# Performance work log

Hardware: AMD Instinct MI355X
Metric: run time of the kernel (lower is better)

The kernel has to match this reference:

```python
import jax, jax.numpy as jnp
import numpy as np

B, S, D, H = 2, 2048, 1024, 16
DK = D // H


def setup_inputs() -> dict:
    key = jax.random.key(0)
    ks = jax.random.split(key, 12)
    scale = 1.0 / np.sqrt(D)
    inp = {
        "q": jax.random.normal(ks[0], (B, S, D), jnp.float32),
        "k": jax.random.normal(ks[1], (B, S, D), jnp.float32),
        "v": jax.random.normal(ks[2], (B, S, D), jnp.float32),
        # causal mask: 1 = attend, 0 = mask, broadcastable to (B, 1, S, S)
        "mask": jnp.tril(jnp.ones((S, S), jnp.int32))[None, None, :, :],
        "Wq": jax.random.normal(ks[3], (D, D), jnp.float32) * scale,
        "bq": jax.random.normal(ks[4], (D,), jnp.float32) * scale,
        "Wk": jax.random.normal(ks[5], (D, D), jnp.float32) * scale,
        "bk": jax.random.normal(ks[6], (D,), jnp.float32) * scale,
        "Wv": jax.random.normal(ks[7], (D, D), jnp.float32) * scale,
        "bv": jax.random.normal(ks[8], (D,), jnp.float32) * scale,
        "Wo": jax.random.normal(ks[9], (D, D), jnp.float32) * scale,
        "bo": jax.random.normal(ks[10], (D,), jnp.float32) * scale,
    }
    return inp


def _split_heads(x):
    b, s, _ = x.shape
    return x.reshape(b, s, H, DK).transpose(0, 2, 1, 3)  # (b, h, s, dk)


def reference(q, k, v, mask, Wq, bq, Wk, bk, Wv, bv, Wo, bo):
    Q = _split_heads(q @ Wq.T + bq)
    K = _split_heads(k @ Wk.T + bk)
    V = _split_heads(v @ Wv.T + bv)
    scores = jnp.einsum("bhqd,bhkd->bhqk", Q, K) * (DK ** -0.5)
    scores = jnp.where(mask == 0, -jnp.inf, scores)
    attn = jax.nn.softmax(scores, axis=-1)  # dropout p=0.0 -> identity
    out = jnp.einsum("bhqk,bhkd->bhqd", attn, V)
    out = out.transpose(0, 2, 1, 3).reshape(q.shape[0], q.shape[1], D)
    return out @ Wo.T + bo
```

## Files before the change

kernel.cpp:

```cpp
#include <hip/hip_runtime.h>


#define S_LEN 2048
#define NHEAD 16
#define DMODEL 1024
#define DKH 64
#define LDT 88

typedef unsigned short u16;
typedef __attribute__((ext_vector_type(4))) short short4v;
typedef __attribute__((ext_vector_type(8))) short short8;
typedef __attribute__((ext_vector_type(8))) __bf16 bf16x8;
typedef __attribute__((ext_vector_type(4))) float f32x4;

__device__ inline u16 f2bf(float f) {
  return __builtin_bit_cast(u16, (__bf16)f);
}

__device__ inline f32x4 mfma16x16(bf16x8 a, bf16x8 b, f32x4 c) {
  return __builtin_amdgcn_mfma_f32_16x16x32_bf16(a, b, c, 0, 0, 0);
}

__device__ inline short8 pack8(float4 a, float4 b) {
  short8 r;
  r[0] = (short)f2bf(a.x); r[1] = (short)f2bf(a.y);
  r[2] = (short)f2bf(a.z); r[3] = (short)f2bf(a.w);
  r[4] = (short)f2bf(b.x); r[5] = (short)f2bf(b.y);
  r[6] = (short)f2bf(b.z); r[7] = (short)f2bf(b.w);
  return r;
}

typedef const __attribute__((address_space(1))) unsigned GU32;
typedef __attribute__((address_space(3))) unsigned LU32;
__device__ inline void gl2lds16(const void* g, void* l) {
  __builtin_amdgcn_global_load_lds((GU32*)g, (LU32*)l, 16, 0, 0);
}

#define SWZ(row, col8) (((row) * 8 + ((col8) ^ ((row) & 7))) * 8)

__global__ __launch_bounds__(256)
void conv_bf16(const float* __restrict__ w0, const float* __restrict__ w1,
               const float* __restrict__ w2, const float* __restrict__ w3,
               const float* __restrict__ aq, const float* __restrict__ ak,
               const float* __restrict__ av,
               u16* __restrict__ o0, u16* __restrict__ o1,
               u16* __restrict__ o2, u16* __restrict__ o3,
               u16* __restrict__ oq, u16* __restrict__ ok, u16* __restrict__ ov)
{
  const int y = blockIdx.y;
  const float* s; u16* d; int n;
  switch (y) {
    case 0: s = w0; d = o0; n = 1 << 20; break;
    case 1: s = w1; d = o1; n = 1 << 20; break;
    case 2: s = w2; d = o2; n = 1 << 20; break;
    case 3: s = w3; d = o3; n = 1 << 20; break;
    case 4: s = aq; d = oq; n = 1 << 22; break;
    case 5: s = ak; d = ok; n = 1 << 22; break;
    default: s = av; d = ov; n = 1 << 22; break;
  }
  const int i = (blockIdx.x * 256 + threadIdx.x) * 8;
  if (i >= n) return;
  float4 a = *(const float4*)&s[i];
  float4 b = *(const float4*)&s[i + 4];
  *(short8*)&d[i] = pack8(a, b);
}

__global__ __launch_bounds__(256)
void conv_w(const float* __restrict__ w0, const float* __restrict__ w1,
            const float* __restrict__ w2, const float* __restrict__ w3,
            u16* __restrict__ o0, u16* __restrict__ o1,
            u16* __restrict__ o2, u16* __restrict__ o3)
{
  const int z = blockIdx.y;
  const float* s = z == 0 ? w0 : z == 1 ? w1 : z == 2 ? w2 : w3;
  u16* d = z == 0 ? o0 : z == 1 ? o1 : z == 2 ? o2 : o3;
  const int i = (blockIdx.x * 256 + threadIdx.x) * 8;
  float4 a = *(const float4*)&s[i];
  float4 b = *(const float4*)&s[i + 4];
  *(short8*)&d[i] = pack8(a, b);
}

__global__ __launch_bounds__(256)
void proj_gemm_bf16(const u16* __restrict__ Aqb, const u16* __restrict__ Akb,
                    const u16* __restrict__ Avb,
                    const u16* __restrict__ Bq, const u16* __restrict__ Bk,
                    const u16* __restrict__ Bv,
                    const float* __restrict__ cq, const float* __restrict__ ck,
                    const float* __restrict__ cv,
                    u16* __restrict__ Oq, u16* __restrict__ Ok, u16* __restrict__ Ov)
{
  __shared__ u16 SM[4 * 8192];

  const int hw = blockIdx.x + (blockIdx.y << 3) + (blockIdx.z << 8);
  const int xcd = hw & 7, sq = hw >> 3;
  const int pan = sq % 12, xb = sq / 12;
  const int p = pan * 8 + xcd;
  const int zz = p >> 5, py = p & 31;

  const u16* Ab = zz == 0 ? Aqb : zz == 1 ? Akb : Avb;
  const u16* Wb = zz == 0 ? Bq : zz == 1 ? Bk : Bv;
  const float* bias = zz == 0 ? cq : zz == 1 ? ck : cv;

  const int t = threadIdx.x;
  const int lane = t & 63;
  const int wv = t >> 6;
  const int wm = wv >> 1, wn = wv & 1;
  const int g = lane >> 4, lr = lane & 15;
  const int bm = py << 7, bn = xb << 7;
  const int K = DMODEL;

  auto STAGE = [&](int buf, int kt) {
    const int k0 = kt << 6;
    u16* Asb = SM + buf * 8192;
    u16* Bsb = SM + 16384 + buf * 8192;
#pragma unroll
    for (int i = 0; i < 4; ++i) {
      int c = t + (i << 8);
      int row = c >> 3, col8 = c & 7;
      int c8s = col8 ^ (row & 7);
      gl2lds16(&Ab[(size_t)(bm + row) * K + k0 + c8s * 8], &Asb[c * 8]);
      gl2lds16(&Wb[(size_t)(bn + row) * K + k0 + c8s * 8], &Bsb[c * 8]);
    }
  };

  f32x4 acc[4][4] = {};
  STAGE(0, 0);
  __syncthreads();
  for (int kt = 0; kt < 16; ++kt) {
    const int cur = kt & 1;
    if (kt + 1 < 16) STAGE(cur ^ 1, kt + 1);
    u16* Asb = SM + cur * 8192;
    u16* Bsb = SM + 16384 + cur * 8192;
    bf16x8 af[2][4], bf[2][4];
#pragma unroll
    for (int kc = 0; kc < 2; ++kc)
#pragma unroll
      for (int f = 0; f < 4; ++f) {
        af[kc][f] = *(const bf16x8*)&Asb[SWZ(wm * 64 + f * 16 + lr, kc * 4 + g)];
        bf[kc][f] = *(const bf16x8*)&Bsb[SWZ(wn * 64 + f * 16 + lr, kc * 4 + g)];
      }
#pragma unroll
    for (int kc = 0; kc < 2; ++kc)
#pragma unroll
      for (int fm = 0; fm < 4; ++fm)
#pragma unroll
        for (int fn = 0; fn < 4; ++fn)
          acc[fm][fn] = mfma16x16(af[kc][fm], bf[kc][fn], acc[fm][fn]);
    __syncthreads();
  }

  if (zz == 2) {
    u16* TL = SM;
    const int b = bm >> 11, s0 = bm & (S_LEN - 1), h0 = bn >> 6;
#pragma unroll
    for (int hh = 0; hh < 2; ++hh) {
      __syncthreads();
      if (wn == hh) {
#pragma unroll
        for (int fm = 0; fm < 4; ++fm)
#pragma unroll
          for (int fn = 0; fn < 4; ++fn) {
            const int lch = fn * 16 + lr;
            const float bb = bias[bn + hh * 64 + lch];
#pragma unroll
            for (int r = 0; r < 4; ++r)
              TL[lch * 132 + wm * 64 + fm * 16 + g * 4 + r] = f2bf(acc[fm][fn][r] + bb);
          }
      }
      __syncthreads();
#pragma unroll
      for (int i = 0; i < 4; ++i) {
        int c = t + (i << 8);
        int dk = c >> 4, sc = (c & 15) << 3;
        short8 vv = *(const short8*)&TL[dk * 132 + sc];
        *(short8*)&Ov[(((size_t)(b * NHEAD + h0 + hh)) * DKH + dk) * S_LEN + s0 + sc] = vv;
      }
    }
  } else {
    u16* Out = zz == 0 ? Oq : Ok;
#pragma unroll
    for (int fm = 0; fm < 4; ++fm)
#pragma unroll
      for (int fn = 0; fn < 4; ++fn) {
        const int col = bn + wn * 64 + fn * 16 + lr;
        const int h = col >> 6, dk = col & (DKH - 1);
        const float bb = bias[col];
#pragma unroll
        for (int r = 0; r < 4; ++r) {
          const int row = bm + wm * 64 + fm * 16 + g * 4 + r;
          const int b = row >> 11, s = row & (S_LEN - 1);
          Out[(((size_t)(b * NHEAD + h)) * S_LEN + s) * DKH + dk] = f2bf(acc[fm][fn][r] + bb);
        }
      }
  }
}

__global__ __launch_bounds__(256)
void proj_gemm_f32(const float* __restrict__ Aq, const float* __restrict__ Akk,
                   const float* __restrict__ Av,
                   const u16* __restrict__ Bq, const u16* __restrict__ Bk,
                   const u16* __restrict__ Bv,
                   const float* __restrict__ cq, const float* __restrict__ ck,
                   const float* __restrict__ cv,
                   u16* __restrict__ Oq, u16* __restrict__ Ok, u16* __restrict__ Ov)
{
  __shared__ u16 SM[3 * 8192];
  u16* As = SM;
  u16* Bs0 = SM + 8192;
  u16* Bs1 = SM + 16384;

  const int hw = blockIdx.x + (blockIdx.y << 3) + (blockIdx.z << 8);
  const int xcd = hw & 7, sq = hw >> 3;
  const int pan = sq % 12, xb = sq / 12;
  const int p = pan * 8 + xcd;
  const int zz = p >> 5, py = p & 31;

  const float* Af = zz == 0 ? Aq : zz == 1 ? Akk : Av;
  const u16* Wb = zz == 0 ? Bq : zz == 1 ? Bk : Bv;
  const float* bias = zz == 0 ? cq : zz == 1 ? ck : cv;

  const int t = threadIdx.x;
  const int lane = t & 63;
  const int wv = t >> 6;
  const int wm = wv >> 1, wn = wv & 1;
  const int g = lane >> 4, lr = lane & 15;
  const int bm = py << 7, bn = xb << 7;
  const int K = DMODEL;

  float4 ax[4], ay[4];
  auto ALOAD = [&](int kt) {
    const int k0 = kt << 6;
#pragma unroll
    for (int i = 0; i < 4; ++i) {
      int c = t + (i << 8);
      int row = c >> 3, col8 = c & 7;
      const float* src = &Af[(size_t)(bm + row) * K + k0 + col8 * 8];
      ax[i] = *(const float4*)src;
      ay[i] = *(const float4*)(src + 4);
    }
  };
  auto AWRITE = [&]() {
#pragma unroll
    for (int i = 0; i < 4; ++i) {
      int c = t + (i << 8);
      int row = c >> 3, col8 = c & 7;
      *(short8*)&As[SWZ(row, col8)] = pack8(ax[i], ay[i]);
    }
  };
  auto BSTAGE = [&](u16* buf, int kt) {
    const int k0 = kt << 6;
#pragma unroll
    for (int i = 0; i < 4; ++i) {
      int c = t + (i << 8);
      int row = c >> 3, col8 = c & 7;
      int c8s = col8 ^ (row & 7);
      gl2lds16(&Wb[(size_t)(bn + row) * K + k0 + c8s * 8], &buf[c * 8]);
    }
  };

  f32x4 acc[4][4] = {};
  ALOAD(0);
  BSTAGE(Bs0, 0);
  AWRITE();
  __syncthreads();
  for (int kt = 0; kt < 16; ++kt) {
    u16* Bcur = (kt & 1) ? Bs1 : Bs0;
    u16* Bnxt = (kt & 1) ? Bs0 : Bs1;
    const bool more = (kt + 1 < 16);
    if (more) { ALOAD(kt + 1); BSTAGE(Bnxt, kt + 1); }
    bf16x8 af[2][4], bf[2][4];
#pragma unroll
    for (int kc = 0; kc < 2; ++kc)
#pragma unroll
      for (int f = 0; f < 4; ++f) {
        af[kc][f] = *(const bf16x8*)&As[SWZ(wm * 64 + f * 16 + lr, kc * 4 + g)];
        bf[kc][f] = *(const bf16x8*)&Bcur[SWZ(wn * 64 + f * 16 + lr, kc * 4 + g)];
      }
#pragma unroll
    for (int kc = 0; kc < 2; ++kc)
#pragma unroll
      for (int fm = 0; fm < 4; ++fm)
#pragma unroll
        for (int fn = 0; fn < 4; ++fn)
          acc[fm][fn] = mfma16x16(af[kc][fm], bf[kc][fn], acc[fm][fn]);
    __syncthreads();
    if (more) {
      AWRITE();
      __syncthreads();
    }
  }

  if (zz == 2) {
    u16* TL = SM;
    const int b = bm >> 11, s0 = bm & (S_LEN - 1), h0 = bn >> 6;
#pragma unroll
    for (int hh = 0; hh < 2; ++hh) {
      __syncthreads();
      if (wn == hh) {
#pragma unroll
        for (int fm = 0; fm < 4; ++fm)
#pragma unroll
          for (int fn = 0; fn < 4; ++fn) {
            const int lch = fn * 16 + lr;
            const float bb = bias[bn + hh * 64 + lch];
#pragma unroll
            for (int r = 0; r < 4; ++r)
              TL[lch * 132 + wm * 64 + fm * 16 + g * 4 + r] = f2bf(acc[fm][fn][r] + bb);
          }
      }
      __syncthreads();
#pragma unroll
      for (int i = 0; i < 4; ++i) {
        int c = t + (i << 8);
        int dk = c >> 4, sc = (c & 15) << 3;
        short8 vv = *(const short8*)&TL[dk * 132 + sc];
        *(short8*)&Ov[(((size_t)(b * NHEAD + h0 + hh)) * DKH + dk) * S_LEN + s0 + sc] = vv;
      }
    }
  } else {
    u16* Out = zz == 0 ? Oq : Ok;
#pragma unroll
    for (int fm = 0; fm < 4; ++fm)
#pragma unroll
      for (int fn = 0; fn < 4; ++fn) {
        const int col = bn + wn * 64 + fn * 16 + lr;
        const int h = col >> 6, dk = col & (DKH - 1);
        const float bb = bias[col];
#pragma unroll
        for (int r = 0; r < 4; ++r) {
          const int row = bm + wm * 64 + fm * 16 + g * 4 + r;
          const int b = row >> 11, s = row & (S_LEN - 1);
          Out[(((size_t)(b * NHEAD + h)) * S_LEN + s) * DKH + dk] = f2bf(acc[fm][fn][r] + bb);
        }
      }
  }
}

__global__ __launch_bounds__(256)
void out_gemm(const u16* __restrict__ Ao, const u16* __restrict__ Wb,
              const float* __restrict__ bias, float* __restrict__ Out)
{
  __shared__ u16 SM[4 * 8192];
  const int hw = blockIdx.x + (blockIdx.y << 3);
  const int xcd = hw & 7, sq = hw >> 3;
  const int pan = sq & 3, xb = sq >> 2;
  const int prow = pan * 8 + xcd;

  const int t = threadIdx.x;
  const int lane = t & 63;
  const int wv = t >> 6;
  const int wm = wv >> 1, wn = wv & 1;
  const int g = lane >> 4, lr = lane & 15;
  const int bm = prow << 7, bn = xb << 7;
  const int K = DMODEL;

  auto STAGE = [&](int buf, int kt) {
    const int k0 = kt << 6;
    u16* Asb = SM + buf * 8192;
    u16* Bsb = SM + 16384 + buf * 8192;
#pragma unroll
    for (int i = 0; i < 4; ++i) {
      int c = t + (i << 8);
      int row = c >> 3, col8 = c & 7;
      int c8s = col8 ^ (row & 7);
      int grow = bm + row;
      int b = grow >> 11, s = grow & (S_LEN - 1);
      int k = k0 + c8s * 8;
      int h = k >> 6, dk = k & (DKH - 1);
      gl2lds16(&Ao[(((size_t)(b * NHEAD + h)) * S_LEN + s) * DKH + dk], &Asb[c * 8]);
      gl2lds16(&Wb[(size_t)(bn + row) * K + k0 + c8s * 8], &Bsb[c * 8]);
    }
  };

  f32x4 acc[4][4] = {};
  STAGE(0, 0);
  __syncthreads();
  for (int kt = 0; kt < 16; ++kt) {
    const int cur = kt & 1;
    if (kt + 1 < 16) STAGE(cur ^ 1, kt + 1);
    u16* Asb = SM + cur * 8192;
    u16* Bsb = SM + 16384 + cur * 8192;
    bf16x8 af[2][4], bf[2][4];
#pragma unroll
    for (int kc = 0; kc < 2; ++kc)
#pragma unroll
      for (int f = 0; f < 4; ++f) {
        af[kc][f] = *(const bf16x8*)&Asb[SWZ(wm * 64 + f * 16 + lr, kc * 4 + g)];
        bf[kc][f] = *(const bf16x8*)&Bsb[SWZ(wn * 64 + f * 16 + lr, kc * 4 + g)];
      }
#pragma unroll
    for (int kc = 0; kc < 2; ++kc)
#pragma unroll
      for (int fm = 0; fm < 4; ++fm)
#pragma unroll
        for (int fn = 0; fn < 4; ++fn)
          acc[fm][fn] = mfma16x16(af[kc][fm], bf[kc][fn], acc[fm][fn]);
    __syncthreads();
  }
#pragma unroll
  for (int fm = 0; fm < 4; ++fm)
#pragma unroll
    for (int fn = 0; fn < 4; ++fn) {
      const int col = bn + wn * 64 + fn * 16 + lr;
      const float bb = bias[col];
#pragma unroll
      for (int r = 0; r < 4; ++r) {
        const int row = bm + wm * 64 + fm * 16 + g * 4 + r;
        Out[(size_t)row * DMODEL + col] = acc[fm][fn][r] + bb;
      }
    }
}

__global__ __launch_bounds__(256)
void attn_fwd(const u16* __restrict__ Qh, const u16* __restrict__ Kh,
              const u16* __restrict__ Vtg, u16* __restrict__ Ao)
{
  __shared__ u16 Ks[2][64 * LDT];
  __shared__ u16 Vs[2][64 * LDT];
  __shared__ u16 Ps[8][16 * LDT];
  const int t = threadIdx.x, lane = t & 63, w = t >> 6;
  const int g = lane >> 4, lr = lane & 15;
  const int bh = blockIdx.y;
  const int pA = blockIdx.x;
  const int tA = pA, tB = 31 - pA;
  const u16* Qb = Qh + (size_t)bh * S_LEN * DKH;
  const u16* Kb = Kh + (size_t)bh * S_LEN * DKH;
  const u16* Vb = Vtg + (size_t)bh * DKH * S_LEN;

  bf16x8 qfA[2], qfB[2];
#pragma unroll
  for (int kc = 0; kc < 2; ++kc) {
    qfA[kc] = *(const bf16x8*)&Qb[(size_t)(tA * 64 + w * 16 + lr) * DKH + kc * 32 + g * 8];
    qfB[kc] = *(const bf16x8*)&Qb[(size_t)(tB * 64 + w * 16 + lr) * DKH + kc * 32 + g * 8];
  }

  f32x4 oA[4] = {}, oB[4] = {};
  float mA = -1e30f, lA = 0.f, mB = -1e30f, lB = 0.f;

  const int r0 = t >> 3;
  const int c0 = (t & 7) << 3;
  short8 kr0, kr1, vr0, vr1;

  auto LOADT = [&](int kt) {
    const int kv0 = kt << 6;
    kr0 = *(const short8*)&Kb[(size_t)(kv0 + r0) * DKH + c0];
    kr1 = *(const short8*)&Kb[(size_t)(kv0 + r0 + 32) * DKH + c0];
    vr0 = *(const short8*)&Vb[(size_t)r0 * S_LEN + kv0 + c0];
    vr1 = *(const short8*)&Vb[(size_t)(r0 + 32) * S_LEN + kv0 + c0];
  };
  auto WRITET = [&](int b) {
    *(short8*)&Ks[b][r0 * LDT + c0] = kr0;
    *(short8*)&Ks[b][(r0 + 32) * LDT + c0] = kr1;
    *(short8*)&Vs[b][r0 * LDT + c0] = vr0;
    *(short8*)&Vs[b][(r0 + 32) * LDT + c0] = vr1;
  };

  auto COMPUTE = [&](int buf, const bf16x8* qf, f32x4* o, float& m, float& l,
                     int pslot, bool diag) {
    f32x4 sf[4];
#pragma unroll
    for (int fk = 0; fk < 4; ++fk) {
      f32x4 a = {};
#pragma unroll
      for (int kc = 0; kc < 2; ++kc) {
        bf16x8 kf = *(const bf16x8*)&Ks[buf][(fk * 16 + lr) * LDT + kc * 32 + g * 8];
        a = mfma16x16(kf, qf[kc], a);
      }
      sf[fk] = a;
    }
    if (diag) {
#pragma unroll
      for (int fk = 0; fk < 4; ++fk)
#pragma unroll
        for (int r = 0; r < 4; ++r)
          if (fk * 16 + 4 * g + r > w * 16 + lr) sf[fk][r] = -1e30f;
    }
    float pm = fmaxf(fmaxf(sf[0][0], sf[0][1]), fmaxf(sf[0][2], sf[0][3]));
#pragma unroll
    for (int fk = 1; fk < 4; ++fk)
      pm = fmaxf(pm, fmaxf(fmaxf(sf[fk][0], sf[fk][1]), fmaxf(sf[fk][2], sf[fk][3])));
    pm = fmaxf(pm, __shfl_xor(pm, 16, 64));
    pm = fmaxf(pm, __shfl_xor(pm, 32, 64));
    float alpha = 1.0f;
    if (!__all(pm - m <= 64.0f)) {
      float mn = fmaxf(m, pm);
      alpha = __expf((m - mn) * 0.125f);
      m = mn;
#pragma unroll
      for (int r = 0; r < 4; ++r) {
        float ar = __shfl(alpha, 4 * g + r, 64);
#pragma unroll
        for (int d = 0; d < 4; ++d) o[d][r] *= ar;
      }
    }
    float rs = 0.f;
#pragma unroll
    for (int fk = 0; fk < 4; ++fk) {
      float p0 = __expf((sf[fk][0] - m) * 0.125f);
      float p1 = __expf((sf[fk][1] - m) * 0.125f);
      float p2 = __expf((sf[fk][2] - m) * 0.125f);
      float p3 = __expf((sf[fk][3] - m) * 0.125f);
      rs += (p0 + p1) + (p2 + p3);
      short4v pk;
      pk[0] = (short)f2bf(p0); pk[1] = (short)f2bf(p1);
      pk[2] = (short)f2bf(p2); pk[3] = (short)f2bf(p3);
      *(short4v*)&Ps[pslot][lr * LDT + fk * 16 + 4 * g] = pk;
    }
    rs += __shfl_xor(rs, 16, 64);
    rs += __shfl_xor(rs, 32, 64);
    l = l * alpha + rs;
#pragma unroll
    for (int kc = 0; kc < 2; ++kc) {
      bf16x8 pf = *(const bf16x8*)&Ps[pslot][lr * LDT + kc * 32 + g * 8];
#pragma unroll
      for (int df = 0; df < 4; ++df) {
        bf16x8 vf = *(const bf16x8*)&Vs[buf][(df * 16 + lr) * LDT + kc * 32 + g * 8];
        o[df] = mfma16x16(pf, vf, o[df]);
      }
    }
  };

  const int nt = tB + 1;
  LOADT(0);
  WRITET(0);
  for (int kt = 0; kt < nt; ++kt) {
    const int cur = kt & 1;
    const bool more = (kt + 1 < nt);
    if (more) LOADT(kt + 1);
    __syncthreads();
    if (kt <= tA) COMPUTE(cur, qfA, oA, mA, lA, w, kt == tA);
    COMPUTE(cur, qfB, oB, mB, lB, 4 + w, kt == tB);
    if (more) WRITET(cur ^ 1);
  }

  float iA[4], iB[4];
#pragma unroll
  for (int r = 0; r < 4; ++r) {
    iA[r] = __builtin_amdgcn_rcpf(__shfl(lA, 4 * g + r, 64));
    iB[r] = __builtin_amdgcn_rcpf(__shfl(lB, 4 * g + r, 64));
  }
#pragma unroll
  for (int df = 0; df < 4; ++df)
#pragma unroll
    for (int r = 0; r < 4; ++r) {
      const int d = df * 16 + lr;
      const int qa = tA * 64 + w * 16 + g * 4 + r;
      const int qb2 = tB * 64 + w * 16 + g * 4 + r;
      Ao[((size_t)bh * S_LEN + qa) * DKH + d] = f2bf(oA[df][r] * iA[r]);
      Ao[((size_t)bh * S_LEN + qb2) * DKH + d] = f2bf(oB[df][r] * iB[r]);
    }
}

extern "C" void kernel_launch(void* const* d_in, const int* in_sizes, int n_in,
                              void* d_out, int out_size, void* d_ws, size_t ws_size,
                              hipStream_t stream)
{
  (void)in_sizes; (void)n_in; (void)out_size;
  const float* q  = (const float*)d_in[0];
  const float* k  = (const float*)d_in[1];
  const float* v  = (const float*)d_in[2];
  const float* Wq = (const float*)d_in[4];
  const float* bq = (const float*)d_in[5];
  const float* Wk = (const float*)d_in[6];
  const float* bk = (const float*)d_in[7];
  const float* Wv = (const float*)d_in[8];
  const float* bv = (const float*)d_in[9];
  const float* Wo = (const float*)d_in[10];
  const float* bo = (const float*)d_in[11];

  char* ws = (char*)d_ws;
  const size_t MB = 1024 * 1024;

  if (ws_size >= 56 * MB) {
    u16* Wqb = (u16*)(ws);
    u16* Wkb = (u16*)(ws + 2 * MB);
    u16* Wvb = (u16*)(ws + 4 * MB);
    u16* Wob = (u16*)(ws + 6 * MB);
    u16* qb  = (u16*)(ws + 8 * MB);
    u16* kb  = (u16*)(ws + 16 * MB);
    u16* vb  = (u16*)(ws + 24 * MB);
    u16* Qh  = (u16*)(ws + 32 * MB);
    u16* Kh  = (u16*)(ws + 40 * MB);
    u16* Vt  = (u16*)(ws + 48 * MB);
    u16* Ao  = qb;

    conv_bf16<<<dim3(2048, 7), 256, 0, stream>>>(Wq, Wk, Wv, Wo, q, k, v,
                                                 Wqb, Wkb, Wvb, Wob, qb, kb, vb);
    proj_gemm_bf16<<<dim3(8, 32, 3), 256, 0, stream>>>(qb, kb, vb, Wqb, Wkb, Wvb,
                                                       bq, bk, bv, Qh, Kh, Vt);
    attn_fwd<<<dim3(16, 2 * NHEAD), 256, 0, stream>>>(Qh, Kh, Vt, Ao);
    out_gemm<<<dim3(8, 32), 256, 0, stream>>>(Ao, Wob, bo, (float*)d_out);
  } else {
    u16* Wqb = (u16*)(ws);
    u16* Wkb = (u16*)(ws + 2 * MB);
    u16* Wvb = (u16*)(ws + 4 * MB);
    u16* Wob = (u16*)(ws + 6 * MB);
    u16* Qh  = (u16*)(ws + 8 * MB);
    u16* Kh  = (u16*)(ws + 16 * MB);
    u16* Vt  = (u16*)(ws + 24 * MB);
    u16* Ao  = (u16*)(ws + 32 * MB);

    conv_w<<<dim3(512, 4), 256, 0, stream>>>(Wq, Wk, Wv, Wo, Wqb, Wkb, Wvb, Wob);
    proj_gemm_f32<<<dim3(8, 32, 3), 256, 0, stream>>>(q, k, v, Wqb, Wkb, Wvb,
                                                      bq, bk, bv, Qh, Kh, Vt);
    attn_fwd<<<dim3(16, 2 * NHEAD), 256, 0, stream>>>(Qh, Kh, Vt, Ao);
    out_gemm<<<dim3(8, 32), 256, 0, stream>>>(Ao, Wob, bo, (float*)d_out);
  }
}
```

Measured before the change: 120.6 us.

## Rework attention kernel with 32x32 MFMA, register-resident P, and split waves per tile

The attention kernel now gives each wave 32 query rows of a single tile (waves 0-1 take tile A, waves 2-3 take tile B) and uses 32x32x16 bf16 MFMA instead of 16x16x32. The softmax probabilities are packed in registers and exchanged across lane halves with shuffles instead of a round trip through a shared-memory P buffer. Exponentials switch to exp2f with the scale folded into a single FMA. Output is staged through LDS so global stores are coalesced. This cuts LDS traffic and instruction count, but waves 0-1 idle once the smaller tile A finishes, which creates per-wave load imbalance.

Result: slower. 145.9 us (+20.9%).

```diff
diff --git a/kernel.cpp b/kernel.cpp
--- a/kernel.cpp
+++ b/kernel.cpp
@@ -5,20 +5,28 @@
 #define NHEAD 16
 #define DMODEL 1024
 #define DKH 64
-#define LDT 88
+#define LDA 72
 
 typedef unsigned short u16;
-typedef __attribute__((ext_vector_type(4))) short short4v;
+typedef unsigned int u32;
 typedef __attribute__((ext_vector_type(8))) short short8;
 typedef __attribute__((ext_vector_type(8))) __bf16 bf16x8;
 typedef __attribute__((ext_vector_type(4))) float f32x4;
+typedef __attribute__((ext_vector_type(16))) float f32x16;
+typedef __attribute__((ext_vector_type(4))) unsigned int u32x4;
 
 __device__ inline u16 f2bf(float f) {
   return __builtin_bit_cast(u16, (__bf16)f);
 }
+__device__ inline u32 pk2(float a, float b) {
+  return (u32)f2bf(a) | ((u32)f2bf(b) << 16);
+}
 
 __device__ inline f32x4 mfma16x16(bf16x8 a, bf16x8 b, f32x4 c) {
   return __builtin_amdgcn_mfma_f32_16x16x32_bf16(a, b, c, 0, 0, 0);
+}
+__device__ inline f32x16 mfma32(bf16x8 a, bf16x8 b, f32x16 c) {
+  return __builtin_amdgcn_mfma_f32_32x32x16_bf16(a, b, c, 0, 0, 0);
 }
 
 __device__ inline short8 pack8(float4 a, float4 b) {
@@ -415,27 +423,26 @@
 void attn_fwd(const u16* __restrict__ Qh, const u16* __restrict__ Kh,
               const u16* __restrict__ Vtg, u16* __restrict__ Ao)
 {
-  __shared__ u16 Ks[2][64 * LDT];
-  __shared__ u16 Vs[2][64 * LDT];
-  __shared__ u16 Ps[8][16 * LDT];
+  __shared__ u16 Ks[2][64 * LDA];
+  __shared__ u16 Vs[2][64 * LDA];
   const int t = threadIdx.x, lane = t & 63, w = t >> 6;
-  const int g = lane >> 4, lr = lane & 15;
+  const int l31 = lane & 31, hi = lane >> 5;
   const int bh = blockIdx.y;
   const int pA = blockIdx.x;
   const int tA = pA, tB = 31 - pA;
+  const int tT = (w < 2) ? tA : tB;
+  const int qg = tT * 64 + (w & 1) * 32 + l31;
   const u16* Qb = Qh + (size_t)bh * S_LEN * DKH;
   const u16* Kb = Kh + (size_t)bh * S_LEN * DKH;
   const u16* Vb = Vtg + (size_t)bh * DKH * S_LEN;
 
-  bf16x8 qfA[2], qfB[2];
-#pragma unroll
-  for (int kc = 0; kc < 2; ++kc) {
-    qfA[kc] = *(const bf16x8*)&Qb[(size_t)(tA * 64 + w * 16 + lr) * DKH + kc * 32 + g * 8];
-    qfB[kc] = *(const bf16x8*)&Qb[(size_t)(tB * 64 + w * 16 + lr) * DKH + kc * 32 + g * 8];
-  }
-
-  f32x4 oA[4] = {}, oB[4] = {};
-  float mA = -1e30f, lA = 0.f, mB = -1e30f, lB = 0.f;
+  bf16x8 qf[4];
+#pragma unroll
+  for (int ks = 0; ks < 4; ++ks)
+    qf[ks] = *(const bf16x8*)&Qb[(size_t)qg * DKH + ks * 16 + 8 * hi];
+
+  f32x16 o0 = {}, o1 = {};
+  float m = -1e30f, l = 0.f;
 
   const int r0 = t >> 3;
   const int c0 = (t & 7) << 3;
@@ -449,77 +456,13 @@
     vr1 = *(const short8*)&Vb[(size_t)(r0 + 32) * S_LEN + kv0 + c0];
   };
   auto WRITET = [&](int b) {
-    *(short8*)&Ks[b][r0 * LDT + c0] = kr0;
-    *(short8*)&Ks[b][(r0 + 32) * LDT + c0] = kr1;
-    *(short8*)&Vs[b][r0 * LDT + c0] = vr0;
-    *(short8*)&Vs[b][(r0 + 32) * LDT + c0] = vr1;
+    *(short8*)&Ks[b][r0 * LDA + c0] = kr0;
+    *(short8*)&Ks[b][(r0 + 32) * LDA + c0] = kr1;
+    *(short8*)&Vs[b][r0 * LDA + c0] = vr0;
+    *(short8*)&Vs[b][(r0 + 32) * LDA + c0] = vr1;
   };
 
-  auto COMPUTE = [&](int buf, const bf16x8* qf, f32x4* o, float& m, float& l,
-                     int pslot, bool diag) {
-    f32x4 sf[4];
-#pragma unroll
-    for (int fk = 0; fk < 4; ++fk) {
-      f32x4 a = {};
-#pragma unroll
-      for (int kc = 0; kc < 2; ++kc) {
-        bf16x8 kf = *(const bf16x8*)&Ks[buf][(fk * 16 + lr) * LDT + kc * 32 + g * 8];
-        a = mfma16x16(kf, qf[kc], a);
-      }
-      sf[fk] = a;
-    }
-    if (diag) {
-#pragma unroll
-      for (int fk = 0; fk < 4; ++fk)
-#pragma unroll
-        for (int r = 0; r < 4; ++r)
-          if (fk * 16 + 4 * g + r > w * 16 + lr) sf[fk][r] = -1e30f;
-    }
-    float pm = fmaxf(fmaxf(sf[0][0], sf[0][1]), fmaxf(sf[0][2], sf[0][3]));
-#pragma unroll
-    for (int fk = 1; fk < 4; ++fk)
-      pm = fmaxf(pm, fmaxf(fmaxf(sf[fk][0], sf[fk][1]), fmaxf(sf[fk][2], sf[fk][3])));
-    pm = fmaxf(pm, __shfl_xor(pm, 16, 64));
-    pm = fmaxf(pm, __shfl_xor(pm, 32, 64));
-    float alpha = 1.0f;
-    if (!__all(pm - m <= 64.0f)) {
-      float mn = fmaxf(m, pm);
-      alpha = __expf((m - mn) * 0.125f);
-      m = mn;
-#pragma unroll
-      for (int r = 0; r < 4; ++r) {
-        float ar = __shfl(alpha, 4 * g + r, 64);
-#pragma unroll
-        for (int d = 0; d < 4; ++d) o[d][r] *= ar;
-      }
-    }
-    float rs = 0.f;
-#pragma unroll
-    for (int fk = 0; fk < 4; ++fk) {
-      float p0 = __expf((sf[fk][0] - m) * 0.125f);
-      float p1 = __expf((sf[fk][1] - m) * 0.125f);
-      float p2 = __expf((sf[fk][2] - m) * 0.125f);
-      float p3 = __expf((sf[fk][3] - m) * 0.125f);
-      rs += (p0 + p1) + (p2 + p3);
-      short4v pk;
-      pk[0] = (short)f2bf(p0); pk[1] = (short)f2bf(p1);
-      pk[2] = (short)f2bf(p2); pk[3] = (short)f2bf(p3);
-      *(short4v*)&Ps[pslot][lr * LDT + fk * 16 + 4 * g] = pk;
-    }
-    rs += __shfl_xor(rs, 16, 64);
-    rs += __shfl_xor(rs, 32, 64);
-    l = l * alpha + rs;
-#pragma unroll
-    for (int kc = 0; kc < 2; ++kc) {
-      bf16x8 pf = *(const bf16x8*)&Ps[pslot][lr * LDT + kc * 32 + g * 8];
-#pragma unroll
-      for (int df = 0; df < 4; ++df) {
-        bf16x8 vf = *(const bf16x8*)&Vs[buf][(df * 16 + lr) * LDT + kc * 32 + g * 8];
-        o[df] = mfma16x16(pf, vf, o[df]);
-      }
-    }
-  };
-
+  const float C2 = 0.18033688011f;
   const int nt = tB + 1;
   LOADT(0);
   WRITET(0);
@@ -528,27 +471,105 @@
     const bool more = (kt + 1 < nt);
     if (more) LOADT(kt + 1);
     __syncthreads();
-    if (kt <= tA) COMPUTE(cur, qfA, oA, mA, lA, w, kt == tA);
-    COMPUTE(cur, qfB, oB, mB, lB, 4 + w, kt == tB);
+    if (w >= 2 || kt <= tA) {
+      f32x16 s0 = {}, s1 = {};
+#pragma unroll
+      for (int ks = 0; ks < 4; ++ks) {
+        bf16x8 k0 = *(const bf16x8*)&Ks[cur][(l31) * LDA + ks * 16 + 8 * hi];
+        bf16x8 k1 = *(const bf16x8*)&Ks[cur][(32 + l31) * LDA + ks * 16 + 8 * hi];
+        s0 = mfma32(k0, qf[ks], s0);
+        s1 = mfma32(k1, qf[ks], s1);
+      }
+      if (kt == tT) {
+        const int kv0 = kt << 6;
+#pragma unroll
+        for (int r = 0; r < 16; ++r) {
+          const int cr = (r & 3) + 8 * (r >> 2) + 4 * hi;
+          if (kv0 + cr > qg) s0[r] = -1e30f;
+          if (kv0 + 32 + cr > qg) s1[r] = -1e30f;
+        }
+      }
+      float pm = fmaxf(s0[0], s0[1]);
+#pragma unroll
+      for (int r = 2; r < 16; ++r) pm = fmaxf(pm, s0[r]);
+#pragma unroll
+      for (int r = 0; r < 16; ++r) pm = fmaxf(pm, s1[r]);
+      pm = fmaxf(pm, __shfl_xor(pm, 32, 64));
+      float alpha = 1.0f;
+      if (!__all(pm - m <= 64.0f)) {
+        const float mn = fmaxf(m, pm);
+        alpha = exp2f((m - mn) * C2);
+        m = mn;
+#pragma unroll
+        for (int r = 0; r < 16; ++r) { o0[r] *= alpha; o1[r] *= alpha; }
+      }
+      const float mC = m * C2;
+      float rs = 0.f;
+#pragma unroll
+      for (int r = 0; r < 16; ++r) {
+        s0[r] = exp2f(fmaf(s0[r], C2, -mC));
+        s1[r] = exp2f(fmaf(s1[r], C2, -mC));
+        rs += s0[r] + s1[r];
+      }
+      rs += __shfl_xor(rs, 32, 64);
+      l = l * alpha + rs;
+      bf16x8 pb[4];
+#pragma unroll
+      for (int s = 0; s < 4; ++s) {
+        const int rb = (s & 1) * 8;
+        float e0, e1, e2, e3, e4, e5, e6, e7;
+        if (s >> 1) {
+          e0 = s1[rb+0]; e1 = s1[rb+1]; e2 = s1[rb+2]; e3 = s1[rb+3];
+          e4 = s1[rb+4]; e5 = s1[rb+5]; e6 = s1[rb+6]; e7 = s1[rb+7];
+        } else {
+          e0 = s0[rb+0]; e1 = s0[rb+1]; e2 = s0[rb+2]; e3 = s0[rb+3];
+          e4 = s0[rb+4]; e5 = s0[rb+5]; e6 = s0[rb+6]; e7 = s0[rb+7];
+        }
+        u32 wlo  = pk2(e0, e1);
+        u32 wlo2 = pk2(e2, e3);
+        u32 whi  = pk2(e4, e5);
+        u32 whi2 = pk2(e6, e7);
+        u32 sA = __shfl_xor(wlo, 32, 64);
+        u32 sB = __shfl_xor(wlo2, 32, 64);
+        u32 sC = __shfl_xor(whi, 32, 64);
+        u32 sD = __shfl_xor(whi2, 32, 64);
+        u32x4 uw;
+        uw[0] = hi ? sC : wlo;
+        uw[1] = hi ? sD : wlo2;
+        uw[2] = hi ? whi : sA;
+        uw[3] = hi ? whi2 : sB;
+        pb[s] = __builtin_bit_cast(bf16x8, uw);
+      }
+#pragma unroll
+      for (int s = 0; s < 4; ++s) {
+        bf16x8 v0 = *(const bf16x8*)&Vs[cur][(l31) * LDA + s * 16 + 8 * hi];
+        bf16x8 v1 = *(const bf16x8*)&Vs[cur][(32 + l31) * LDA + s * 16 + 8 * hi];
+        o0 = mfma32(v0, pb[s], o0);
+        o1 = mfma32(v1, pb[s], o1);
+      }
+    }
     if (more) WRITET(cur ^ 1);
   }
 
-  float iA[4], iB[4];
-#pragma unroll
-  for (int r = 0; r < 4; ++r) {
-    iA[r] = __builtin_amdgcn_rcpf(__shfl(lA, 4 * g + r, 64));
-    iB[r] = __builtin_amdgcn_rcpf(__shfl(lB, 4 * g + r, 64));
-  }
-#pragma unroll
-  for (int df = 0; df < 4; ++df)
-#pragma unroll
-    for (int r = 0; r < 4; ++r) {
-      const int d = df * 16 + lr;
-      const int qa = tA * 64 + w * 16 + g * 4 + r;
-      const int qb2 = tB * 64 + w * 16 + g * 4 + r;
-      Ao[((size_t)bh * S_LEN + qa) * DKH + d] = f2bf(oA[df][r] * iA[r]);
-      Ao[((size_t)bh * S_LEN + qb2) * DKH + d] = f2bf(oB[df][r] * iB[r]);
-    }
+  const float il = __builtin_amdgcn_rcpf(l);
+  __syncthreads();
+  u16* Os = (w < 2) ? Ks[0] : Ks[1];
+  const int rl = (w & 1) * 32 + l31;
+#pragma unroll
+  for (int r = 0; r < 16; ++r) {
+    const int cr = (r & 3) + 8 * (r >> 2) + 4 * hi;
+    Os[rl * LDA + cr] = f2bf(o0[r] * il);
+    Os[rl * LDA + 32 + cr] = f2bf(o1[r] * il);
+  }
+  __syncthreads();
+#pragma unroll
+  for (int i = 0; i < 2; ++i) {
+    const int rr = r0 + i * 32;
+    *(short8*)&Ao[((size_t)bh * S_LEN + tA * 64 + rr) * DKH + c0] =
+        *(const short8*)&Ks[0][rr * LDA + c0];
+    *(short8*)&Ao[((size_t)bh * S_LEN + tB * 64 + rr) * DKH + c0] =
+        *(const short8*)&Ks[1][rr * LDA + c0];
+  }
 }
 
 extern "C" void kernel_launch(void* const* d_in, const int* in_sizes, int n_in,
```

## Swizzle K/V shared tiles, use exp2 with folded scale, add MFMA priority hints

Applied to the files above, without the earlier changes.

Replaces the padded K/V LDS tiles (stride 88) with dense 64-wide tiles whose 16-byte slots are XOR-swizzled by row, cutting LDS footprint and aiming to avoid bank conflicts on fragment reads. Softmax exponentials switch from __expf with a 0.125 scale to exp2f with the log2e-folded constant, computed as a single fma per element. It also raises wave priority around the MFMA sections with s_setprio. The swizzle must match on write and read, and the priority hints may or may not help scheduling.

Measured after the change: 124.1 us. +2.9%, slower.

```diff
diff --git a/kernel.cpp b/kernel.cpp
--- a/kernel.cpp
+++ b/kernel.cpp
@@ -411,12 +411,13 @@
     }
 }
 
+#define KSW(row, slot) (((row) << 6) + ((((slot) ^ ((row) & 7))) << 3))
 __global__ __launch_bounds__(256)
 void attn_fwd(const u16* __restrict__ Qh, const u16* __restrict__ Kh,
               const u16* __restrict__ Vtg, u16* __restrict__ Ao)
 {
-  __shared__ u16 Ks[2][64 * LDT];
-  __shared__ u16 Vs[2][64 * LDT];
+  __shared__ u16 Ks[2][64 * 64];
+  __shared__ u16 Vs[2][64 * 64];
   __shared__ u16 Ps[8][16 * LDT];
   const int t = threadIdx.x, lane = t & 63, w = t >> 6;
   const int g = lane >> 4, lr = lane & 15;
@@ -438,36 +439,41 @@
   float mA = -1e30f, lA = 0.f, mB = -1e30f, lB = 0.f;
 
   const int r0 = t >> 3;
-  const int c0 = (t & 7) << 3;
+  const int sl0 = t & 7;
   short8 kr0, kr1, vr0, vr1;
 
   auto LOADT = [&](int kt) {
     const int kv0 = kt << 6;
+    const int c0 = sl0 << 3;
     kr0 = *(const short8*)&Kb[(size_t)(kv0 + r0) * DKH + c0];
     kr1 = *(const short8*)&Kb[(size_t)(kv0 + r0 + 32) * DKH + c0];
     vr0 = *(const short8*)&Vb[(size_t)r0 * S_LEN + kv0 + c0];
     vr1 = *(const short8*)&Vb[(size_t)(r0 + 32) * S_LEN + kv0 + c0];
   };
   auto WRITET = [&](int b) {
-    *(short8*)&Ks[b][r0 * LDT + c0] = kr0;
-    *(short8*)&Ks[b][(r0 + 32) * LDT + c0] = kr1;
-    *(short8*)&Vs[b][r0 * LDT + c0] = vr0;
-    *(short8*)&Vs[b][(r0 + 32) * LDT + c0] = vr1;
-  };
+    *(short8*)&Ks[b][KSW(r0, sl0)] = kr0;
+    *(short8*)&Ks[b][KSW(r0 + 32, sl0)] = kr1;
+    *(short8*)&Vs[b][KSW(r0, sl0)] = vr0;
+    *(short8*)&Vs[b][KSW(r0 + 32, sl0)] = vr1;
+  };
+
+  const float C2 = 0.18033688011f;
 
   auto COMPUTE = [&](int buf, const bf16x8* qf, f32x4* o, float& m, float& l,
                      int pslot, bool diag) {
     f32x4 sf[4];
+    __builtin_amdgcn_s_setprio(1);
 #pragma unroll
     for (int fk = 0; fk < 4; ++fk) {
       f32x4 a = {};
 #pragma unroll
       for (int kc = 0; kc < 2; ++kc) {
-        bf16x8 kf = *(const bf16x8*)&Ks[buf][(fk * 16 + lr) * LDT + kc * 32 + g * 8];
+        bf16x8 kf = *(const bf16x8*)&Ks[buf][KSW(fk * 16 + lr, kc * 4 + g)];
         a = mfma16x16(kf, qf[kc], a);
       }
       sf[fk] = a;
     }
+    __builtin_amdgcn_s_setprio(0);
     if (diag) {
 #pragma unroll
       for (int fk = 0; fk < 4; ++fk)
@@ -484,7 +490,7 @@
     float alpha = 1.0f;
     if (!__all(pm - m <= 64.0f)) {
       float mn = fmaxf(m, pm);
-      alpha = __expf((m - mn) * 0.125f);
+      alpha = exp2f((m - mn) * C2);
       m = mn;
 #pragma unroll
       for (int r = 0; r < 4; ++r) {
@@ -493,13 +499,14 @@
         for (int d = 0; d < 4; ++d) o[d][r] *= ar;
       }
     }
+    const float mC = m * C2;
     float rs = 0.f;
 #pragma unroll
     for (int fk = 0; fk < 4; ++fk) {
-      float p0 = __expf((sf[fk][0] - m) * 0.125f);
-      float p1 = __expf((sf[fk][1] - m) * 0.125f);
-      float p2 = __expf((sf[fk][2] - m) * 0.125f);
-      float p3 = __expf((sf[fk][3] - m) * 0.125f);
+      float p0 = exp2f(fmaf(sf[fk][0], C2, -mC));
+      float p1 = exp2f(fmaf(sf[fk][1], C2, -mC));
+      float p2 = exp2f(fmaf(sf[fk][2], C2, -mC));
+      float p3 = exp2f(fmaf(sf[fk][3], C2, -mC));
       rs += (p0 + p1) + (p2 + p3);
       short4v pk;
       pk[0] = (short)f2bf(p0); pk[1] = (short)f2bf(p1);
@@ -512,11 +519,13 @@
 #pragma unroll
     for (int kc = 0; kc < 2; ++kc) {
       bf16x8 pf = *(const bf16x8*)&Ps[pslot][lr * LDT + kc * 32 + g * 8];
+      __builtin_amdgcn_s_setprio(1);
 #pragma unroll
       for (int df = 0; df < 4; ++df) {
-        bf16x8 vf = *(const bf16x8*)&Vs[buf][(df * 16 + lr) * LDT + kc * 32 + g * 8];
+        bf16x8 vf = *(const bf16x8*)&Vs[buf][KSW(df * 16 + lr, kc * 4 + g)];
         o[df] = mfma16x16(pf, vf, o[df]);
       }
+      __builtin_amdgcn_s_setprio(0);
     }
   };
 
```
